# Kernel tuning notes

Measured on AMD Instinct MI355X. Metric: run time of the kernel, lower is better.

Reference implementation:

```python
import jax, jax.numpy as jnp
import numpy as np

B = 4096  # batch of 28x28 grayscale images


def setup_inputs() -> dict:
    key = jax.random.key(0)
    k1, k2, k3 = jax.random.split(key, 3)
    x = jax.random.uniform(k1, (B, 28, 28), jnp.float32)
    # 5 trainable rotation angles of the fixed 'RandomLayer' circuit
    rand_params = jax.random.uniform(k2, (5,), jnp.float32, 0.0, 2.0 * np.pi)
    W = jax.random.normal(k3, (10, 4 * 14 * 14), jnp.float32) * 0.02
    b = jnp.zeros((10,), jnp.float32)
    return {"x": x, "rand_params": rand_params, "W": W, "b": b}


def _apply1(state, U, w):
    # state: (N,2,2,2,2) complex; apply 2x2 gate U on wire w
    st = jnp.moveaxis(state, w + 1, -1)
    st = st @ U.T
    return jnp.moveaxis(st, -1, w + 1)


def _apply2(state, U, w1, w2):
    # apply 4x4 gate U on (w1,w2), w1 < w2
    st = jnp.moveaxis(state, (w1 + 1, w2 + 1), (-2, -1))
    shp = st.shape
    st = st.reshape(shp[:-2] + (4,)) @ U.T
    return jnp.moveaxis(st.reshape(shp), (-2, -1), (w1 + 1, w2 + 1))


def _ry(t):
    c = jnp.cos(t / 2).astype(jnp.complex64)
    s = jnp.sin(t / 2).astype(jnp.complex64)
    return jnp.stack([jnp.stack([c, -s]), jnp.stack([s, c])])


def _rx(t):
    c = jnp.cos(t / 2).astype(jnp.complex64)
    s = jnp.sin(t / 2).astype(jnp.complex64)
    return jnp.stack([jnp.stack([c, -1j * s]), jnp.stack([-1j * s, c])])


def _rz(t):
    e = jnp.exp(-0.5j * t).astype(jnp.complex64)
    z = jnp.zeros((), jnp.complex64)
    return jnp.stack([jnp.stack([e, z]), jnp.stack([z, jnp.conj(e)])])


_CNOT = jnp.array([[1, 0, 0, 0], [0, 1, 0, 0], [0, 0, 0, 1], [0, 0, 1, 0]], jnp.complex64)


def _forward(x, rand_params, W, b):
    bsz = x.shape[0]
    # 2x2 patches in row-major (r,c) order; pixel order (r,c),(r,c+1),(r+1,c),(r+1,c+1)
    xp = x.reshape(bsz, 14, 2, 14, 2).transpose(0, 1, 3, 2, 4).reshape(bsz, 196, 4)
    ang = xp.reshape(-1, 4)  # (N,4) angles, N = bsz*196
    c, s = jnp.cos(ang / 2), jnp.sin(ang / 2)
    # Ry(theta_i)|0> on each wire => product state built via einsum
    a = [jnp.stack([c[:, i], s[:, i]], axis=-1) for i in range(4)]
    state = jnp.einsum('na,nb,nc,nd->nabcd', a[0], a[1], a[2], a[3]).astype(jnp.complex64)
    # fixed 8-op 'RandomLayer' circuit
    state = _apply1(state, _ry(rand_params[0]), 0)
    state = _apply1(state, _rx(rand_params[1]), 1)
    state = _apply2(state, _CNOT, 0, 1)
    state = _apply1(state, _rz(rand_params[2]), 2)
    state = _apply1(state, _ry(rand_params[3]), 3)
    state = _apply2(state, _CNOT, 2, 3)
    state = _apply1(state, _rx(rand_params[4]), 0)
    state = _apply2(state, _CNOT, 1, 2)
    # PauliZ expectation per wire
    probs = state.real ** 2 + state.imag ** 2  # (N,2,2,2,2)
    z = jnp.array([1.0, -1.0], jnp.float32)
    ez = [jnp.einsum('nabcd,a->n', probs, z),
          jnp.einsum('nabcd,b->n', probs, z),
          jnp.einsum('nabcd,c->n', probs, z),
          jnp.einsum('nabcd,d->n', probs, z)]
    feats = jnp.stack(ez, axis=-1).reshape(bsz, 196 * 4)
    logits = feats @ W.T + b
    return jax.nn.log_softmax(logits, axis=-1)


def reference(x, rand_params, W, b):
    return _forward(x, rand_params, W, b)
```

## Files before the change

kernel.cpp:

```cpp
#include <hip/hip_runtime.h>
#include <math.h>


#define RY_GATE(bit, c_, s_) do {                                          \
    _Pragma("unroll")                                                      \
    for (int j = 0; j < 8; ++j) {                                          \
        const int lo = ((j >> (bit)) << ((bit) + 1)) | (j & ((1 << (bit)) - 1)); \
        const int hi = lo | (1 << (bit));                                  \
        float u0r = sr[lo], u0i = si[lo], u1r = sr[hi], u1i = si[hi];      \
        sr[lo] = (c_) * u0r - (s_) * u1r; si[lo] = (c_) * u0i - (s_) * u1i; \
        sr[hi] = (s_) * u0r + (c_) * u1r; si[hi] = (s_) * u0i + (c_) * u1i; \
    }                                                                      \
} while (0)

#define RX_GATE(bit, c_, s_) do {                                          \
    _Pragma("unroll")                                                      \
    for (int j = 0; j < 8; ++j) {                                          \
        const int lo = ((j >> (bit)) << ((bit) + 1)) | (j & ((1 << (bit)) - 1)); \
        const int hi = lo | (1 << (bit));                                  \
        float u0r = sr[lo], u0i = si[lo], u1r = sr[hi], u1i = si[hi];      \
        sr[lo] = (c_) * u0r + (s_) * u1i; si[lo] = (c_) * u0i - (s_) * u1r; \
        sr[hi] = (c_) * u1r + (s_) * u0i; si[hi] = (c_) * u1i - (s_) * u0r; \
    }                                                                      \
} while (0)

#define RZ_GATE(bit, c_, s_) do {                                          \
    _Pragma("unroll")                                                      \
    for (int j = 0; j < 8; ++j) {                                          \
        const int lo = ((j >> (bit)) << ((bit) + 1)) | (j & ((1 << (bit)) - 1)); \
        const int hi = lo | (1 << (bit));                                  \
        float r0 = sr[lo], i0 = si[lo], r1 = sr[hi], i1 = si[hi];          \
        sr[lo] = (c_) * r0 + (s_) * i0; si[lo] = (c_) * i0 - (s_) * r0;    \
        sr[hi] = (c_) * r1 - (s_) * i1; si[hi] = (c_) * i1 + (s_) * r1;    \
    }                                                                      \
} while (0)

#define CNOT_GATE(cb, tb) do {                                             \
    _Pragma("unroll")                                                      \
    for (int idx = 0; idx < 16; ++idx) {                                   \
        if (((idx >> (cb)) & 1) && !((idx >> (tb)) & 1)) {                 \
            const int o = idx | (1 << (tb));                               \
            float tr = sr[idx], ti = si[idx];                              \
            sr[idx] = sr[o]; si[idx] = si[o];                              \
            sr[o] = tr;      si[o] = ti;                                   \
        }                                                                  \
    }                                                                      \
} while (0)

__device__ __forceinline__ void sim_patch(const float ang[4],
                                          const float gc[5], const float gs[5],
                                          float ez[4])
{
    float ca[4], sa[4];
#pragma unroll
    for (int i = 0; i < 4; ++i) __sincosf(0.5f * ang[i], &sa[i], &ca[i]);

    float ab[4] = { ca[0] * ca[1], ca[0] * sa[1], sa[0] * ca[1], sa[0] * sa[1] };
    float cd[4] = { ca[2] * ca[3], ca[2] * sa[3], sa[2] * ca[3], sa[2] * sa[3] };
    float sr[16], si[16];
#pragma unroll
    for (int h = 0; h < 4; ++h)
#pragma unroll
        for (int l = 0; l < 4; ++l)
            sr[h * 4 + l] = ab[h] * cd[l];

#pragma unroll
    for (int j = 0; j < 8; ++j) {
        const int lo = j, hi = j | 8;
        float t0 = sr[lo], t1 = sr[hi];
        sr[lo] = gc[0] * t0 - gs[0] * t1;
        sr[hi] = gs[0] * t0 + gc[0] * t1;
    }
#pragma unroll
    for (int j = 0; j < 8; ++j) {
        const int lo = ((j >> 2) << 3) | (j & 3);
        const int hi = lo | 4;
        float t0 = sr[lo], t1 = sr[hi];
        sr[lo] = gc[1] * t0;  si[lo] = -gs[1] * t1;
        sr[hi] = gc[1] * t1;  si[hi] = -gs[1] * t0;
    }
    CNOT_GATE(3, 2);
    RZ_GATE(1, gc[2], gs[2]);
    RY_GATE(0, gc[3], gs[3]);
    CNOT_GATE(1, 0);
    RX_GATE(3, gc[4], gs[4]);
    CNOT_GATE(2, 1);

    float p[16];
#pragma unroll
    for (int i = 0; i < 16; ++i)
        p[i] = fmaf(sr[i], sr[i], si[i] * si[i]);

    float S0 = 0.f, S1 = 0.f, S2 = 0.f, S3 = 0.f;
#pragma unroll
    for (int i = 0; i < 16; ++i) {
        if (i & 8) S0 += p[i];
        if (i & 4) S1 += p[i];
        if (i & 2) S2 += p[i];
        if (i & 1) S3 += p[i];
    }
    ez[0] = fmaf(-2.f, S0, 1.f);
    ez[1] = fmaf(-2.f, S1, 1.f);
    ez[2] = fmaf(-2.f, S2, 1.f);
    ez[3] = fmaf(-2.f, S3, 1.f);
}

__global__ __launch_bounds__(256, 4) void quanv_fused_kernel(
    const float* __restrict__ x,
    const float* __restrict__ rp,
    const float* __restrict__ W,
    const float* __restrict__ bias,
    float* __restrict__ out)
{
    const int tid  = threadIdx.x;
    const int lane = tid & 63;
    const int img  = (blockIdx.x << 2) + (tid >> 6);

    float gc[5], gs[5];
#pragma unroll
    for (int i = 0; i < 5; ++i) __sincosf(0.5f * rp[i], &gs[i], &gc[i]);

    float acc[10];
#pragma unroll
    for (int c = 0; c < 10; ++c) acc[c] = 0.0f;

    const float* xb = x + (size_t)img * 784;

#pragma unroll 1
    for (int k = 0; k < 4; ++k) {
        const int pidx = lane + (k << 6);
        if (pidx < 196) {
            const int pr = pidx / 14;
            const int pc = pidx - pr * 14;
            const float* px = xb + pr * 56 + pc * 2;
            const float2 r0 = *(const float2*)(px);
            const float2 r1 = *(const float2*)(px + 28);
            const float ang[4] = { r0.x, r0.y, r1.x, r1.y };

            float ez[4];
            sim_patch(ang, gc, gs, ez);

#pragma unroll
            for (int c = 0; c < 10; ++c) {
                const float4 wv = *(const float4*)(W + c * 784 + pidx * 4);
                acc[c] = fmaf(wv.x, ez[0],
                         fmaf(wv.y, ez[1],
                         fmaf(wv.z, ez[2],
                         fmaf(wv.w, ez[3], acc[c]))));
            }
        }
    }

#pragma unroll
    for (int c = 0; c < 10; ++c) {
        float v = acc[c];
#pragma unroll
        for (int off = 32; off > 0; off >>= 1) v += __shfl_xor(v, off, 64);
        acc[c] = v + bias[c];
    }

    float m = acc[0];
#pragma unroll
    for (int c = 1; c < 10; ++c) m = fmaxf(m, acc[c]);
    float s = 0.0f;
#pragma unroll
    for (int c = 0; c < 10; ++c) s += __expf(acc[c] - m);
    const float lse = m + __logf(s);

    float myv = acc[0];
#pragma unroll
    for (int c = 1; c < 10; ++c) myv = (lane == c) ? acc[c] : myv;
    if (lane < 10) out[(size_t)img * 10 + lane] = myv - lse;
}

extern "C" void kernel_launch(void* const* d_in, const int* in_sizes, int n_in,
                              void* d_out, int out_size, void* d_ws, size_t ws_size,
                              hipStream_t stream) {
    const float* x    = (const float*)d_in[0];
    const float* rp   = (const float*)d_in[1];
    const float* W    = (const float*)d_in[2];
    const float* bias = (const float*)d_in[3];
    float* out = (float*)d_out;

    quanv_fused_kernel<<<1024, 256, 0, stream>>>(x, rp, W, bias, out);
}
```

Baseline: 78.09 us.

## Replace per-patch statevector simulation with closed-form PauliZ expectations

The explicit 16-amplitude complex statevector simulation of the fixed circuit is replaced by an analytic closed form. Each wire's Z expectation becomes a product of cosines of input angles shifted by the rotation parameters. This removes most of the per-patch ALU work and registers, and the patch loop is now fully unrolled. Correctness depends on the derived identity holding for this exact gate sequence. The RZ parameter drops out, which is valid since it commutes with Z measurement.

```diff
diff --git a/kernel.cpp b/kernel.cpp
--- a/kernel.cpp
+++ b/kernel.cpp
@@ -1,109 +1,6 @@
 #include <hip/hip_runtime.h>
 #include <math.h>
 
-
-#define RY_GATE(bit, c_, s_) do {                                          \
-    _Pragma("unroll")                                                      \
-    for (int j = 0; j < 8; ++j) {                                          \
-        const int lo = ((j >> (bit)) << ((bit) + 1)) | (j & ((1 << (bit)) - 1)); \
-        const int hi = lo | (1 << (bit));                                  \
-        float u0r = sr[lo], u0i = si[lo], u1r = sr[hi], u1i = si[hi];      \
-        sr[lo] = (c_) * u0r - (s_) * u1r; si[lo] = (c_) * u0i - (s_) * u1i; \
-        sr[hi] = (s_) * u0r + (c_) * u1r; si[hi] = (s_) * u0i + (c_) * u1i; \
-    }                                                                      \
-} while (0)
-
-#define RX_GATE(bit, c_, s_) do {                                          \
-    _Pragma("unroll")                                                      \
-    for (int j = 0; j < 8; ++j) {                                          \
-        const int lo = ((j >> (bit)) << ((bit) + 1)) | (j & ((1 << (bit)) - 1)); \
-        const int hi = lo | (1 << (bit));                                  \
-        float u0r = sr[lo], u0i = si[lo], u1r = sr[hi], u1i = si[hi];      \
-        sr[lo] = (c_) * u0r + (s_) * u1i; si[lo] = (c_) * u0i - (s_) * u1r; \
-        sr[hi] = (c_) * u1r + (s_) * u0i; si[hi] = (c_) * u1i - (s_) * u0r; \
-    }                                                                      \
-} while (0)
-
-#define RZ_GATE(bit, c_, s_) do {                                          \
-    _Pragma("unroll")                                                      \
-    for (int j = 0; j < 8; ++j) {                                          \
-        const int lo = ((j >> (bit)) << ((bit) + 1)) | (j & ((1 << (bit)) - 1)); \
-        const int hi = lo | (1 << (bit));                                  \
-        float r0 = sr[lo], i0 = si[lo], r1 = sr[hi], i1 = si[hi];          \
-        sr[lo] = (c_) * r0 + (s_) * i0; si[lo] = (c_) * i0 - (s_) * r0;    \
-        sr[hi] = (c_) * r1 - (s_) * i1; si[hi] = (c_) * i1 + (s_) * r1;    \
-    }                                                                      \
-} while (0)
-
-#define CNOT_GATE(cb, tb) do {                                             \
-    _Pragma("unroll")                                                      \
-    for (int idx = 0; idx < 16; ++idx) {                                   \
-        if (((idx >> (cb)) & 1) && !((idx >> (tb)) & 1)) {                 \
-            const int o = idx | (1 << (tb));                               \
-            float tr = sr[idx], ti = si[idx];                              \
-            sr[idx] = sr[o]; si[idx] = si[o];                              \
-            sr[o] = tr;      si[o] = ti;                                   \
-        }                                                                  \
-    }                                                                      \
-} while (0)
-
-__device__ __forceinline__ void sim_patch(const float ang[4],
-                                          const float gc[5], const float gs[5],
-                                          float ez[4])
-{
-    float ca[4], sa[4];
-#pragma unroll
-    for (int i = 0; i < 4; ++i) __sincosf(0.5f * ang[i], &sa[i], &ca[i]);
-
-    float ab[4] = { ca[0] * ca[1], ca[0] * sa[1], sa[0] * ca[1], sa[0] * sa[1] };
-    float cd[4] = { ca[2] * ca[3], ca[2] * sa[3], sa[2] * ca[3], sa[2] * sa[3] };
-    float sr[16], si[16];
-#pragma unroll
-    for (int h = 0; h < 4; ++h)
-#pragma unroll
-        for (int l = 0; l < 4; ++l)
-            sr[h * 4 + l] = ab[h] * cd[l];
-
-#pragma unroll
-    for (int j = 0; j < 8; ++j) {
-        const int lo = j, hi = j | 8;
-        float t0 = sr[lo], t1 = sr[hi];
-        sr[lo] = gc[0] * t0 - gs[0] * t1;
-        sr[hi] = gs[0] * t0 + gc[0] * t1;
-    }
-#pragma unroll
-    for (int j = 0; j < 8; ++j) {
-        const int lo = ((j >> 2) << 3) | (j & 3);
-        const int hi = lo | 4;
-        float t0 = sr[lo], t1 = sr[hi];
-        sr[lo] = gc[1] * t0;  si[lo] = -gs[1] * t1;
-        sr[hi] = gc[1] * t1;  si[hi] = -gs[1] * t0;
-    }
-    CNOT_GATE(3, 2);
-    RZ_GATE(1, gc[2], gs[2]);
-    RY_GATE(0, gc[3], gs[3]);
-    CNOT_GATE(1, 0);
-    RX_GATE(3, gc[4], gs[4]);
-    CNOT_GATE(2, 1);
-
-    float p[16];
-#pragma unroll
-    for (int i = 0; i < 16; ++i)
-        p[i] = fmaf(sr[i], sr[i], si[i] * si[i]);
-
-    float S0 = 0.f, S1 = 0.f, S2 = 0.f, S3 = 0.f;
-#pragma unroll
-    for (int i = 0; i < 16; ++i) {
-        if (i & 8) S0 += p[i];
-        if (i & 4) S1 += p[i];
-        if (i & 2) S2 += p[i];
-        if (i & 1) S3 += p[i];
-    }
-    ez[0] = fmaf(-2.f, S0, 1.f);
-    ez[1] = fmaf(-2.f, S1, 1.f);
-    ez[2] = fmaf(-2.f, S2, 1.f);
-    ez[3] = fmaf(-2.f, S3, 1.f);
-}
 
 __global__ __launch_bounds__(256, 4) void quanv_fused_kernel(
     const float* __restrict__ x,
@@ -116,9 +13,10 @@
     const int lane = tid & 63;
     const int img  = (blockIdx.x << 2) + (tid >> 6);
 
-    float gc[5], gs[5];
-#pragma unroll
-    for (int i = 0; i < 5; ++i) __sincosf(0.5f * rp[i], &gs[i], &gc[i]);
+    const float p0  = rp[0];
+    const float cp1 = __cosf(rp[1]);
+    const float p3  = rp[3];
+    const float cp4 = __cosf(rp[4]);
 
     float acc[10];
 #pragma unroll
@@ -126,7 +24,7 @@
 
     const float* xb = x + (size_t)img * 784;
 
-#pragma unroll 1
+#pragma unroll
     for (int k = 0; k < 4; ++k) {
         const int pidx = lane + (k << 6);
         if (pidx < 196) {
@@ -135,18 +33,24 @@
             const float* px = xb + pr * 56 + pc * 2;
             const float2 r0 = *(const float2*)(px);
             const float2 r1 = *(const float2*)(px + 28);
-            const float ang[4] = { r0.x, r0.y, r1.x, r1.y };
 
-            float ez[4];
-            sim_patch(ang, gc, gs, ez);
+            const float z0 = __cosf(r0.x + p0);
+            const float z1 = __cosf(r0.y);
+            const float z2 = __cosf(r1.x);
+            const float z3 = __cosf(r1.y + p3);
+
+            const float ez0 = cp4 * z0;
+            const float ez1 = cp1 * z0 * z1;
+            const float ez2 = ez1 * z2;
+            const float ez3 = z2 * z3;
 
 #pragma unroll
             for (int c = 0; c < 10; ++c) {
                 const float4 wv = *(const float4*)(W + c * 784 + pidx * 4);
-                acc[c] = fmaf(wv.x, ez[0],
-                         fmaf(wv.y, ez[1],
-                         fmaf(wv.z, ez[2],
-                         fmaf(wv.w, ez[3], acc[c]))));
+                acc[c] = fmaf(wv.x, ez0,
+                         fmaf(wv.y, ez1,
+                         fmaf(wv.z, ez2,
+                         fmaf(wv.w, ez3, acc[c]))));
             }
         }
     }
```

Result: faster. 71.29 us (-8.7%).
